# Kernel tuning notes

Hardware: AMD Instinct MI355X
Metric: run time of the kernel (lower is better)

Reference implementation:

```python
import jax, jax.numpy as jnp
import numpy as np

DIM = 128
NUM_HEADS = 8
HEAD_DIM = DIM // NUM_HEADS
N_NODES = 50000
N_EDGES = 800000


def setup_inputs() -> dict:
    key = jax.random.key(0)
    ks = jax.random.split(key, 10)
    scale = 1.0 / np.sqrt(DIM)
    x = jax.random.normal(ks[0], (N_NODES, DIM), dtype=jnp.float32)
    edge_index = jax.random.randint(ks[1], (2, N_EDGES), 0, N_NODES, dtype=jnp.int64)
    Wq = jax.random.normal(ks[2], (DIM, DIM), dtype=jnp.float32) * scale
    bq = jnp.zeros((DIM,), dtype=jnp.float32)
    Wk = jax.random.normal(ks[3], (DIM, DIM), dtype=jnp.float32) * scale
    bk = jnp.zeros((DIM,), dtype=jnp.float32)
    Wv = jax.random.normal(ks[4], (DIM, DIM), dtype=jnp.float32) * scale
    bv = jnp.zeros((DIM,), dtype=jnp.float32)
    Wo = jax.random.normal(ks[5], (DIM, DIM), dtype=jnp.float32) * scale
    bo = jnp.zeros((DIM,), dtype=jnp.float32)
    return {"x": x, "edge_index": edge_index, "Wq": Wq, "bq": bq,
            "Wk": Wk, "bk": bk, "Wv": Wv, "bv": bv, "Wo": Wo, "bo": bo}


def reference(x, edge_index, Wq, bq, Wk, bk, Wv, bv, Wo, bo):
    n = x.shape[0]
    tgt = edge_index[0]  # softmax group / scatter destination
    src = edge_index[1]  # gather source
    # projections: torch nn.Linear -> x @ W.T + b
    q = (x @ Wq.T + bq).reshape(n, NUM_HEADS, HEAD_DIM)
    k = (x @ Wk.T + bk).reshape(n, NUM_HEADS, HEAD_DIM)
    v = (x @ Wv.T + bv).reshape(n, NUM_HEADS, HEAD_DIM)
    # edge-wise attention scores: [E, H]
    scores = jnp.einsum('ehd,ehd->eh', q[src], k[tgt]) / np.sqrt(HEAD_DIM).astype(np.float32)
    # segment softmax over edges grouped by target node
    m = jax.ops.segment_max(scores, tgt, num_segments=n)          # [N, H]
    m = jax.lax.stop_gradient(m)
    p = jnp.exp(scores - m[tgt])                                   # [E, H]
    s = jax.ops.segment_sum(p, tgt, num_segments=n)               # [N, H]
    probs = p / s[tgt]
    # weighted scatter-add of source values
    weighted = v[src] * probs[..., None]                           # [E, H, D]
    agg = jax.ops.segment_sum(weighted, tgt, num_segments=n)      # [N, H, D]
    out = agg.reshape(n, DIM) @ Wo.T + bo
    # dropout is identity in eval mode
    return out
```

## Files before the change

kernel.cpp:

```cpp
#include <hip/hip_runtime.h>
#include <math.h>

#define NN 50000
#define NE 800000
#define DIM 128
#define NH 8
#define HD 16
#define NTILE 3125
#define TPB 782
#define LROW 136
#define QVROW 256
#define SCAN_B 196

typedef short v8s __attribute__((ext_vector_type(8)));
typedef float v4f __attribute__((ext_vector_type(4)));

__device__ __forceinline__ unsigned short f2b(float f) {
    unsigned u = __float_as_uint(f);
    u = (u + 0x7fffu + ((u >> 16) & 1u)) >> 16;
    return (unsigned short)u;
}
__device__ __forceinline__ float blo(unsigned w) { return __uint_as_float(w << 16); }
__device__ __forceinline__ float bhi(unsigned w) { return __uint_as_float(w & 0xffff0000u); }

#define NW4 (4 * DIM * DIM / 4)
#define NC4 ((NN + 3) / 4)
__global__ __launch_bounds__(256) void convert_kernel(
    const float* __restrict__ Wq, const float* __restrict__ Wk,
    const float* __restrict__ Wv, const float* __restrict__ Wo,
    unsigned short* __restrict__ Wb, int* __restrict__ cnt)
{
    int i = blockIdx.x * 256 + threadIdx.x;
    if (i < NW4) {
        int mat = i >> 12;
        int off = i & 4095;
        const float* Wsrc = (mat == 0) ? Wq : (mat == 1) ? Wk : (mat == 2) ? Wv : Wo;
        float4 f = ((const float4*)Wsrc)[off];
        uint2 o;
        o.x = (unsigned)f2b(f.x) | ((unsigned)f2b(f.y) << 16);
        o.y = (unsigned)f2b(f.z) | ((unsigned)f2b(f.w) << 16);
        ((uint2*)(Wb + (size_t)mat * DIM * DIM))[off] = o;
    } else if (i < NW4 + NC4) {
        ((int4*)cnt)[i - NW4] = make_int4(0, 0, 0, 0);
    }
}

__global__ __launch_bounds__(256) void qkv_mfma_kernel(
    const float* __restrict__ x, const unsigned short* __restrict__ Wb,
    const float* __restrict__ bq, const float* __restrict__ bk, const float* __restrict__ bv,
    unsigned short* __restrict__ qvb, unsigned short* __restrict__ kb,
    const int* __restrict__ tgt, int* __restrict__ cnt)
{
    __shared__ unsigned short Wl[DIM * LROW];
    const int mat = blockIdx.x / TPB;
    const int tg  = blockIdx.x % TPB;
    const int tid = threadIdx.x;
    const int lane = tid & 63;
    const int warp = tid >> 6;
    const int m = lane & 15;
    const int quad = lane >> 4;

    const int gsize = 3 * TPB * 256;
    for (int e = blockIdx.x * 256 + tid; e < NE; e += gsize)
        atomicAdd(cnt + tgt[e], 1);

    const unsigned short* Wg = Wb + (size_t)mat * DIM * DIM;
#pragma unroll
    for (int it = 0; it < 8; ++it) {
        int chunk = it * 256 + tid;
        int row = chunk >> 4, c8 = chunk & 15;
        *(uint4*)(Wl + row * LROW + c8 * 8) = ((const uint4*)Wg)[chunk];
    }
    __syncthreads();

    const int rt = tg * 4 + warp;
    if (rt >= NTILE) return;
    const int r0 = rt * 16;

    const float* bias_p = (mat == 0) ? bq : (mat == 1) ? bk : bv;

    v8s a[4];
#pragma unroll
    for (int kt = 0; kt < 4; ++kt) {
        const float4* xr = (const float4*)(x + (size_t)(r0 + m) * DIM + kt * 32 + quad * 8);
        float4 f0 = xr[0], f1 = xr[1];
        v8s t;
        t[0] = (short)f2b(f0.x); t[1] = (short)f2b(f0.y);
        t[2] = (short)f2b(f0.z); t[3] = (short)f2b(f0.w);
        t[4] = (short)f2b(f1.x); t[5] = (short)f2b(f1.y);
        t[6] = (short)f2b(f1.z); t[7] = (short)f2b(f1.w);
        a[kt] = t;
    }

#pragma unroll
    for (int nt = 0; nt < 8; ++nt) {
        v4f c = {0.f, 0.f, 0.f, 0.f};
#pragma unroll
        for (int kt = 0; kt < 4; ++kt) {
            v8s b = *(const v8s*)(Wl + (nt * 16 + m) * LROW + kt * 32 + quad * 8);
            c = __builtin_amdgcn_mfma_f32_16x16x32_bf16(a[kt], b, c, 0, 0, 0);
        }
        int col = nt * 16 + m;
        float bias = bias_p[col];
#pragma unroll
        for (int i = 0; i < 4; ++i) {
            int row = r0 + quad * 4 + i;
            unsigned short val = f2b(c[i] + bias);
            if (mat == 1) {
                kb[(size_t)row * DIM + col] = val;
            } else {
                int pos = (col >> 1) * 4 + (col & 1) + ((mat == 2) ? 2 : 0);
                qvb[(size_t)row * QVROW + pos] = val;
            }
        }
    }
}

__global__ __launch_bounds__(256) void scan1_kernel(
    const int* __restrict__ cnt, int* __restrict__ off, int* __restrict__ bsum)
{
    __shared__ int ws4[4];
    const int tid = threadIdx.x, lane = tid & 63, wid = tid >> 6;
    int i = blockIdx.x * 256 + tid;
    int v0 = (i < NN) ? cnt[i] : 0;
    int incl = v0;
#pragma unroll
    for (int d = 1; d < 64; d <<= 1) {
        int t = __shfl_up(incl, d);
        if (lane >= d) incl += t;
    }
    if (lane == 63) ws4[wid] = incl;
    __syncthreads();
    int wexcl = 0;
#pragma unroll
    for (int t = 0; t < 3; ++t) if (t < wid) wexcl += ws4[t];
    if (i < NN) off[i] = wexcl + incl - v0;
    if (tid == 255) bsum[blockIdx.x] = wexcl + incl;
}

__global__ __launch_bounds__(256) void scan23_kernel(
    const int* __restrict__ bsum, int* __restrict__ off, int* __restrict__ cursor)
{
    __shared__ int ws4[4];
    __shared__ int base_s, total_s;
    const int tid = threadIdx.x, lane = tid & 63, wid = tid >> 6;
    int v0 = (tid < SCAN_B) ? bsum[tid] : 0;
    int incl = v0;
#pragma unroll
    for (int d = 1; d < 64; d <<= 1) {
        int t = __shfl_up(incl, d);
        if (lane >= d) incl += t;
    }
    if (lane == 63) ws4[wid] = incl;
    __syncthreads();
    int wexcl = 0;
#pragma unroll
    for (int t = 0; t < 3; ++t) if (t < wid) wexcl += ws4[t];
    int excl = wexcl + incl - v0;
    if (tid == blockIdx.x) base_s = excl;
    if (tid == SCAN_B - 1) total_s = excl + v0;
    __syncthreads();
    int i = blockIdx.x * 256 + tid;
    if (i < NN) {
        int t = off[i] + base_s;
        off[i] = t;
        cursor[i] = t;
    }
    if (blockIdx.x == SCAN_B - 1 && tid == 0) off[NN] = total_s;
}

__global__ __launch_bounds__(256) void fill_kernel(
    const int* __restrict__ tgt, const int* __restrict__ src,
    int* __restrict__ cursor, int* __restrict__ edge_src)
{
    int e = blockIdx.x * 256 + threadIdx.x;
    if (e >= NE) return;
    int t = tgt[e];
    int pos = atomicAdd(cursor + t, 1);
    edge_src[pos] = src[e];
}

__global__ __launch_bounds__(256) void attn_kernel(
    const int* __restrict__ off, const int* __restrict__ edge_src,
    const unsigned short* __restrict__ qvb, const unsigned short* __restrict__ kb,
    unsigned short* __restrict__ aggb)
{
    __shared__ float red[2][64][3];
    const int tid = threadIdx.x;
    const int nib = tid >> 7;
    const int w   = (tid >> 6) & 1;
    const int lane = tid & 63;
    const int node = blockIdx.x * 2 + nib;

    const int base = off[node];
    const int deg  = off[node + 1] - base;

    unsigned kw = *(const unsigned*)(kb + (size_t)node * DIM + 2 * lane);
    const float klo = blo(kw), khi = bhi(kw);

    const int j = lane & 7;
    const int gb = lane & 56;

    float ax = 0.f, ay = 0.f, ss = 0.f;
    const int nw = (deg + 1 - w) >> 1;
    for (int c0 = 0; c0 < nw; c0 += 64) {
        int idx = c0 + lane;
        int srcv = edge_src[base + min(2 * idx + w, deg - 1)];
        int nchunk = min(nw - c0, 64);
        for (int b = 0; b < nchunk; b += 8) {
            int nb = min(nchunk - b, 8);
            uint2 qv[8];
#pragma unroll
            for (int i = 0; i < 8; ++i) {
                int si = __shfl(srcv, b + min(i, nb - 1));
                qv[i] = *(const uint2*)(qvb + (size_t)si * QVROW + 4 * lane);
            }
            float part[8];
#pragma unroll
            for (int i = 0; i < 8; ++i)
                part[i] = blo(qv[i].x) * klo + bhi(qv[i].x) * khi;
            float r1[4];
#pragma unroll
            for (int t = 0; t < 4; ++t) {
                float keep = (j & 1) ? part[2 * t + 1] : part[2 * t];
                float send = (j & 1) ? part[2 * t]     : part[2 * t + 1];
                r1[t] = keep + __shfl_xor(send, 1);
            }
            float r2[2];
#pragma unroll
            for (int u = 0; u < 2; ++u) {
                float keep = (j & 2) ? r1[2 * u + 1] : r1[2 * u];
                float send = (j & 2) ? r1[2 * u]     : r1[2 * u + 1];
                r2[u] = keep + __shfl_xor(send, 2);
            }
            float keep = (j & 4) ? r2[1] : r2[0];
            float send = (j & 4) ? r2[0] : r2[1];
            float tot = keep + __shfl_xor(send, 4);
            float p = __expf(tot * 0.25f);
#pragma unroll
            for (int i = 0; i < 8; ++i) {
                if (i < nb) {
                    float pi = __shfl(p, gb + i);
                    unsigned vv = qv[i].y;
                    ax += pi * blo(vv);
                    ay += pi * bhi(vv);
                    ss += pi;
                }
            }
        }
    }
    if (w == 1) {
        red[nib][lane][0] = ax; red[nib][lane][1] = ay; red[nib][lane][2] = ss;
    }
    __syncthreads();
    if (w == 0) {
        ax += red[nib][lane][0]; ay += red[nib][lane][1]; ss += red[nib][lane][2];
        unsigned* ap = (unsigned*)(aggb + (size_t)node * DIM + 2 * lane);
        if (deg == 0) {
            *ap = 0u;
        } else {
            float inv = 1.f / ss;
            *ap = (unsigned)f2b(ax * inv) | ((unsigned)f2b(ay * inv) << 16);
        }
    }
}

__global__ __launch_bounds__(256) void outproj_mfma_kernel(
    const unsigned short* __restrict__ aggb, const unsigned short* __restrict__ Wob,
    const float* __restrict__ bo, float* __restrict__ out)
{
    __shared__ unsigned short Wl[DIM * LROW];
    const int tid = threadIdx.x;
    const int lane = tid & 63;
    const int warp = tid >> 6;
    const int m = lane & 15;
    const int quad = lane >> 4;

#pragma unroll
    for (int it = 0; it < 8; ++it) {
        int chunk = it * 256 + tid;
        int row = chunk >> 4, c8 = chunk & 15;
        *(uint4*)(Wl + row * LROW + c8 * 8) = ((const uint4*)Wob)[chunk];
    }
    __syncthreads();

    const int rt = blockIdx.x * 4 + warp;
    if (rt >= NTILE) return;
    const int r0 = rt * 16;

    v8s a[4];
#pragma unroll
    for (int kt = 0; kt < 4; ++kt)
        a[kt] = *(const v8s*)(aggb + (size_t)(r0 + m) * DIM + kt * 32 + quad * 8);

#pragma unroll
    for (int nt = 0; nt < 8; ++nt) {
        v4f c = {0.f, 0.f, 0.f, 0.f};
#pragma unroll
        for (int kt = 0; kt < 4; ++kt) {
            v8s b = *(const v8s*)(Wl + (nt * 16 + m) * LROW + kt * 32 + quad * 8);
            c = __builtin_amdgcn_mfma_f32_16x16x32_bf16(a[kt], b, c, 0, 0, 0);
        }
        int col = nt * 16 + m;
        float bias = bo[col];
#pragma unroll
        for (int i = 0; i < 4; ++i) {
            int row = r0 + quad * 4 + i;
            out[(size_t)row * DIM + col] = c[i] + bias;
        }
    }
}

extern "C" void kernel_launch(void* const* d_in, const int* in_sizes, int n_in,
                              void* d_out, int out_size, void* d_ws, size_t ws_size,
                              hipStream_t stream) {
    const float* x  = (const float*)d_in[0];
    const int*   ei = (const int*)d_in[1];
    const float* Wq = (const float*)d_in[2];
    const float* bq = (const float*)d_in[3];
    const float* Wk = (const float*)d_in[4];
    const float* bk = (const float*)d_in[5];
    const float* Wv = (const float*)d_in[6];
    const float* bv = (const float*)d_in[7];
    const float* Wo = (const float*)d_in[8];
    const float* bo = (const float*)d_in[9];

    const int* tgt = ei;
    const int* src = ei + NE;

    char* ws = (char*)d_ws;
    const size_t SZ_QV = (size_t)NN * QVROW * 2;
    const size_t SZ_BF = (size_t)NN * DIM * 2;

    unsigned short* qvb  = (unsigned short*)(ws);
    unsigned short* kb   = (unsigned short*)(ws + SZ_QV);
    unsigned short* aggb = (unsigned short*)(ws + SZ_QV + SZ_BF);
    unsigned short* Wb   = (unsigned short*)(ws + SZ_QV + 2 * SZ_BF);

    char* wi = ws + SZ_QV + 2 * SZ_BF + (size_t)4 * DIM * DIM * 2;
    int* cnt      = (int*)(wi);
    int* off      = (int*)(wi + (size_t)NN * 4);
    int* cursor   = (int*)(wi + (size_t)(2 * NN + 1) * 4);
    int* edge_src = (int*)(wi + (size_t)(3 * NN + 1) * 4);
    int* bsum     = (int*)(wi + (size_t)(3 * NN + 1) * 4 + (size_t)NE * 4);

    const int conv_blocks = (NW4 + NC4 + 255) / 256;
    const int edge_blocks = (NE + 255) / 256;

    convert_kernel<<<conv_blocks, 256, 0, stream>>>(Wq, Wk, Wv, Wo, Wb, cnt);
    qkv_mfma_kernel<<<3 * TPB, 256, 0, stream>>>(x, Wb, bq, bk, bv, qvb, kb, tgt, cnt);
    scan1_kernel<<<SCAN_B, 256, 0, stream>>>(cnt, off, bsum);
    scan23_kernel<<<SCAN_B, 256, 0, stream>>>(bsum, off, cursor);
    fill_kernel<<<edge_blocks, 256, 0, stream>>>(tgt, src, cursor, edge_src);
    attn_kernel<<<(NN + 1) / 2, 256, 0, stream>>>(off, edge_src, qvb, kb, aggb);
    outproj_mfma_kernel<<<TPB, 256, 0, stream>>>(
        aggb, Wb + (size_t)3 * DIM * DIM, bo, (float*)d_out);
}
```

Before: 251.5 us.

## Fuse QKV matrices per block and use one wavefront per node in attention

The QKV projection now has each block loop over all three weight matrices, so each x tile is loaded and converted to bf16 once instead of three times, at the cost of extra syncs and weight reloads into LDS. The attention kernel drops the two-wavefront-per-node split and its LDS reduction, mapping one wavefront to each node. Cross-lane shuffles become ds_swizzle and readlane, and the node offsets become wave-uniform via readfirstlane. The sum of probabilities is kept per lane and reduced only at the end, which trades some per-node parallelism for less shuffle and sync overhead.

```diff
diff --git a/kernel.cpp b/kernel.cpp
--- a/kernel.cpp
+++ b/kernel.cpp
@@ -22,6 +22,11 @@
 }
 __device__ __forceinline__ float blo(unsigned w) { return __uint_as_float(w << 16); }
 __device__ __forceinline__ float bhi(unsigned w) { return __uint_as_float(w & 0xffff0000u); }
+
+template<int PAT>
+__device__ __forceinline__ float swz(float x) {
+    return __int_as_float(__builtin_amdgcn_ds_swizzle(__float_as_int(x), PAT));
+}
 
 #define NW4 (4 * DIM * DIM / 4)
 #define NC4 ((NN + 3) / 4)
@@ -52,65 +57,70 @@
     const int* __restrict__ tgt, int* __restrict__ cnt)
 {
     __shared__ unsigned short Wl[DIM * LROW];
-    const int mat = blockIdx.x / TPB;
-    const int tg  = blockIdx.x % TPB;
     const int tid = threadIdx.x;
     const int lane = tid & 63;
     const int warp = tid >> 6;
     const int m = lane & 15;
     const int quad = lane >> 4;
 
-    const int gsize = 3 * TPB * 256;
+    const int gsize = TPB * 256;
     for (int e = blockIdx.x * 256 + tid; e < NE; e += gsize)
         atomicAdd(cnt + tgt[e], 1);
 
-    const unsigned short* Wg = Wb + (size_t)mat * DIM * DIM;
-#pragma unroll
-    for (int it = 0; it < 8; ++it) {
-        int chunk = it * 256 + tid;
-        int row = chunk >> 4, c8 = chunk & 15;
-        *(uint4*)(Wl + row * LROW + c8 * 8) = ((const uint4*)Wg)[chunk];
-    }
-    __syncthreads();
-
-    const int rt = tg * 4 + warp;
-    if (rt >= NTILE) return;
+    const int rt = blockIdx.x * 4 + warp;
     const int r0 = rt * 16;
-
-    const float* bias_p = (mat == 0) ? bq : (mat == 1) ? bk : bv;
+    const bool act = (rt < NTILE);
 
     v8s a[4];
-#pragma unroll
-    for (int kt = 0; kt < 4; ++kt) {
-        const float4* xr = (const float4*)(x + (size_t)(r0 + m) * DIM + kt * 32 + quad * 8);
-        float4 f0 = xr[0], f1 = xr[1];
-        v8s t;
-        t[0] = (short)f2b(f0.x); t[1] = (short)f2b(f0.y);
-        t[2] = (short)f2b(f0.z); t[3] = (short)f2b(f0.w);
-        t[4] = (short)f2b(f1.x); t[5] = (short)f2b(f1.y);
-        t[6] = (short)f2b(f1.z); t[7] = (short)f2b(f1.w);
-        a[kt] = t;
-    }
-
-#pragma unroll
-    for (int nt = 0; nt < 8; ++nt) {
-        v4f c = {0.f, 0.f, 0.f, 0.f};
+    if (act) {
 #pragma unroll
         for (int kt = 0; kt < 4; ++kt) {
-            v8s b = *(const v8s*)(Wl + (nt * 16 + m) * LROW + kt * 32 + quad * 8);
-            c = __builtin_amdgcn_mfma_f32_16x16x32_bf16(a[kt], b, c, 0, 0, 0);
-        }
-        int col = nt * 16 + m;
-        float bias = bias_p[col];
-#pragma unroll
-        for (int i = 0; i < 4; ++i) {
-            int row = r0 + quad * 4 + i;
-            unsigned short val = f2b(c[i] + bias);
-            if (mat == 1) {
-                kb[(size_t)row * DIM + col] = val;
-            } else {
-                int pos = (col >> 1) * 4 + (col & 1) + ((mat == 2) ? 2 : 0);
-                qvb[(size_t)row * QVROW + pos] = val;
+            const float4* xr = (const float4*)(x + (size_t)(r0 + m) * DIM + kt * 32 + quad * 8);
+            float4 f0 = xr[0], f1 = xr[1];
+            v8s t;
+            t[0] = (short)f2b(f0.x); t[1] = (short)f2b(f0.y);
+            t[2] = (short)f2b(f0.z); t[3] = (short)f2b(f0.w);
+            t[4] = (short)f2b(f1.x); t[5] = (short)f2b(f1.y);
+            t[6] = (short)f2b(f1.z); t[7] = (short)f2b(f1.w);
+            a[kt] = t;
+        }
+    }
+
+#pragma unroll
+    for (int mat = 0; mat < 3; ++mat) {
+        if (mat) __syncthreads();
+        const unsigned short* Wg = Wb + (size_t)mat * DIM * DIM;
+#pragma unroll
+        for (int it = 0; it < 8; ++it) {
+            int chunk = it * 256 + tid;
+            int row = chunk >> 4, c8 = chunk & 15;
+            *(uint4*)(Wl + row * LROW + c8 * 8) = ((const uint4*)Wg)[chunk];
+        }
+        __syncthreads();
+
+        if (act) {
+            const float* bias_p = (mat == 0) ? bq : (mat == 1) ? bk : bv;
+#pragma unroll
+            for (int nt = 0; nt < 8; ++nt) {
+                v4f c = {0.f, 0.f, 0.f, 0.f};
+#pragma unroll
+                for (int kt = 0; kt < 4; ++kt) {
+                    v8s b = *(const v8s*)(Wl + (nt * 16 + m) * LROW + kt * 32 + quad * 8);
+                    c = __builtin_amdgcn_mfma_f32_16x16x32_bf16(a[kt], b, c, 0, 0, 0);
+                }
+                int col = nt * 16 + m;
+                float bias = bias_p[col];
+#pragma unroll
+                for (int i = 0; i < 4; ++i) {
+                    int row = r0 + quad * 4 + i;
+                    unsigned short val = f2b(c[i] + bias);
+                    if (mat == 1) {
+                        kb[(size_t)row * DIM + col] = val;
+                    } else {
+                        int pos = (col >> 1) * 4 + (col & 1) + ((mat == 2) ? 2 : 0);
+                        qvb[(size_t)row * QVROW + pos] = val;
+                    }
+                }
             }
         }
     }
@@ -185,35 +195,30 @@
     const unsigned short* __restrict__ qvb, const unsigned short* __restrict__ kb,
     unsigned short* __restrict__ aggb)
 {
-    __shared__ float red[2][64][3];
     const int tid = threadIdx.x;
-    const int nib = tid >> 7;
-    const int w   = (tid >> 6) & 1;
     const int lane = tid & 63;
-    const int node = blockIdx.x * 2 + nib;
-
-    const int base = off[node];
-    const int deg  = off[node + 1] - base;
+    const int node = blockIdx.x * 4 + (tid >> 6);
+    if (node >= NN) return;
+
+    const int base = __builtin_amdgcn_readfirstlane(off[node]);
+    const int deg  = __builtin_amdgcn_readfirstlane(off[node + 1]) - base;
 
     unsigned kw = *(const unsigned*)(kb + (size_t)node * DIM + 2 * lane);
     const float klo = blo(kw), khi = bhi(kw);
-
     const int j = lane & 7;
-    const int gb = lane & 56;
 
     float ax = 0.f, ay = 0.f, ss = 0.f;
-    const int nw = (deg + 1 - w) >> 1;
-    for (int c0 = 0; c0 < nw; c0 += 64) {
-        int idx = c0 + lane;
-        int srcv = edge_src[base + min(2 * idx + w, deg - 1)];
-        int nchunk = min(nw - c0, 64);
+
+    for (int c0 = 0; c0 < deg; c0 += 64) {
+        const int nchunk = min(deg - c0, 64);
+        int srcv = edge_src[base + c0 + min(lane, nchunk - 1)];
         for (int b = 0; b < nchunk; b += 8) {
-            int nb = min(nchunk - b, 8);
+            const int nb = min(nchunk - b, 8);
             uint2 qv[8];
 #pragma unroll
             for (int i = 0; i < 8; ++i) {
-                int si = __shfl(srcv, b + min(i, nb - 1));
-                qv[i] = *(const uint2*)(qvb + (size_t)si * QVROW + 4 * lane);
+                int si = __builtin_amdgcn_readlane(srcv, min(b + i, nchunk - 1));
+                qv[i] = ((const uint2*)(qvb + (size_t)si * QVROW))[lane];
             }
             float part[8];
 #pragma unroll
@@ -224,44 +229,36 @@
             for (int t = 0; t < 4; ++t) {
                 float keep = (j & 1) ? part[2 * t + 1] : part[2 * t];
                 float send = (j & 1) ? part[2 * t]     : part[2 * t + 1];
-                r1[t] = keep + __shfl_xor(send, 1);
+                r1[t] = keep + swz<0x041F>(send);
             }
             float r2[2];
 #pragma unroll
             for (int u = 0; u < 2; ++u) {
                 float keep = (j & 2) ? r1[2 * u + 1] : r1[2 * u];
                 float send = (j & 2) ? r1[2 * u]     : r1[2 * u + 1];
-                r2[u] = keep + __shfl_xor(send, 2);
+                r2[u] = keep + swz<0x081F>(send);
             }
             float keep = (j & 4) ? r2[1] : r2[0];
             float send = (j & 4) ? r2[0] : r2[1];
-            float tot = keep + __shfl_xor(send, 4);
-            float p = __expf(tot * 0.25f);
-#pragma unroll
-            for (int i = 0; i < 8; ++i) {
-                if (i < nb) {
-                    float pi = __shfl(p, gb + i);
-                    unsigned vv = qv[i].y;
-                    ax += pi * blo(vv);
-                    ay += pi * bhi(vv);
-                    ss += pi;
-                }
-            }
-        }
-    }
-    if (w == 1) {
-        red[nib][lane][0] = ax; red[nib][lane][1] = ay; red[nib][lane][2] = ss;
-    }
-    __syncthreads();
-    if (w == 0) {
-        ax += red[nib][lane][0]; ay += red[nib][lane][1]; ss += red[nib][lane][2];
-        unsigned* ap = (unsigned*)(aggb + (size_t)node * DIM + 2 * lane);
-        if (deg == 0) {
-            *ap = 0u;
-        } else {
-            float inv = 1.f / ss;
-            *ap = (unsigned)f2b(ax * inv) | ((unsigned)f2b(ay * inv) << 16);
-        }
+            float tot = keep + swz<0x101F>(send);
+            float p = (j < nb) ? __expf(tot * 0.25f) : 0.f;
+            ss += p;
+#define ACC(i) { float pi = swz<((i) << 5) | 0x18>(p); unsigned vv = qv[i].y; \
+                 ax += pi * blo(vv); ay += pi * bhi(vv); }
+            ACC(0) ACC(1) ACC(2) ACC(3) ACC(4) ACC(5) ACC(6) ACC(7)
+#undef ACC
+        }
+    }
+    ss += swz<0x041F>(ss);
+    ss += swz<0x081F>(ss);
+    ss += swz<0x101F>(ss);
+
+    unsigned* ap = (unsigned*)(aggb + (size_t)node * DIM + 2 * lane);
+    if (deg == 0) {
+        *ap = 0u;
+    } else {
+        float inv = 1.f / ss;
+        *ap = (unsigned)f2b(ax * inv) | ((unsigned)f2b(ay * inv) << 16);
     }
 }
 
@@ -348,11 +345,11 @@
     const int edge_blocks = (NE + 255) / 256;
 
     convert_kernel<<<conv_blocks, 256, 0, stream>>>(Wq, Wk, Wv, Wo, Wb, cnt);
-    qkv_mfma_kernel<<<3 * TPB, 256, 0, stream>>>(x, Wb, bq, bk, bv, qvb, kb, tgt, cnt);
+    qkv_mfma_kernel<<<TPB, 256, 0, stream>>>(x, Wb, bq, bk, bv, qvb, kb, tgt, cnt);
     scan1_kernel<<<SCAN_B, 256, 0, stream>>>(cnt, off, bsum);
     scan23_kernel<<<SCAN_B, 256, 0, stream>>>(bsum, off, cursor);
     fill_kernel<<<edge_blocks, 256, 0, stream>>>(tgt, src, cursor, edge_src);
-    attn_kernel<<<(NN + 1) / 2, 256, 0, stream>>>(off, edge_src, qvb, kb, aggb);
+    attn_kernel<<<(NN + 3) / 4, 256, 0, stream>>>(off, edge_src, qvb, kb, aggb);
     outproj_mfma_kernel<<<TPB, 256, 0, stream>>>(
         aggb, Wb + (size_t)3 * DIM * DIM, bo, (float*)d_out);
 }
```

Result: no change. 253.1 us (+0.6%).
